# Performance work log

Measured on AMD Instinct MI355X. Metric: run time of the kernel, lower is better.

Reference implementation:

```python
import jax, jax.numpy as jnp
import numpy as np

N_USERS = 200000
N_MOVIES = 80000
N = N_USERS + N_MOVIES
H = 64
F_MOVIE = 20
E = 1250000
EL = 500000


def setup_inputs() -> dict:
    key = jax.random.key(0)
    ks = jax.random.split(key, 13)
    s = 0.05
    inp = {
        "movie_x": jax.random.normal(ks[0], (N_MOVIES, F_MOVIE), jnp.float32),
        "user_emb": jax.random.normal(ks[1], (N_USERS, H), jnp.float32) * s,
        "movie_emb": jax.random.normal(ks[2], (N_MOVIES, H), jnp.float32) * s,
        "lin_W": jax.random.normal(ks[3], (H, F_MOVIE), jnp.float32) * s,
        "lin_b": jax.random.normal(ks[4], (H,), jnp.float32) * s,
        "W1l": jax.random.normal(ks[5], (H, H), jnp.float32) * s,
        "b1": jax.random.normal(ks[6], (H,), jnp.float32) * s,
        "W1r": jax.random.normal(ks[7], (H, H), jnp.float32) * s,
        "W2l": jax.random.normal(ks[8], (H, H), jnp.float32) * s,
        "b2": jax.random.normal(ks[9], (H,), jnp.float32) * s,
        "W2r": jax.random.normal(ks[10], (H, H), jnp.float32) * s,
        "edge_index": jax.random.randint(ks[11], (2, E), 0, N, jnp.int64),
        "edge_label_index": jnp.stack([
            jax.random.randint(jax.random.fold_in(ks[12], 0), (EL,), 0, N_USERS, jnp.int64),
            jax.random.randint(jax.random.fold_in(ks[12], 1), (EL,), 0, N_MOVIES, jnp.int64),
        ]),
    }
    return inp


def _sage(x, src, dst, Wl, bl, Wr):
    # PyG SAGEConv, mean aggregation: lin_l(mean_{j->i} x_j) + lin_r(x_i)
    msg = x[src]  # [E, H] gather
    agg = jax.ops.segment_sum(msg, dst, num_segments=N)  # [N, H] scatter-add
    deg = jax.ops.segment_sum(jnp.ones((src.shape[0],), x.dtype), dst, num_segments=N)
    mean = agg / jnp.maximum(deg, 1.0)[:, None]
    return mean @ Wl.T + bl + x @ Wr.T


def reference(movie_x, user_emb, movie_emb, lin_W, lin_b,
              W1l, b1, W1r, W2l, b2, W2r, edge_index, edge_label_index):
    # encode: users = embedding lookup (node_id == arange), movies = linear(x) + embedding
    x_user = user_emb
    x_movie = movie_x @ lin_W.T + lin_b + movie_emb
    x = jnp.concatenate([x_user, x_movie], axis=0)  # [N, H]

    src, dst = edge_index[0], edge_index[1]
    x = jax.nn.relu(_sage(x, src, dst, W1l, b1, W1r))
    x = _sage(x, src, dst, W2l, b2, W2r)

    xu = x[:N_USERS]
    xm = x[N_USERS:]
    # dot-product edge scoring over supervision edges
    u = xu[edge_label_index[0]]  # [EL, H]
    m = xm[edge_label_index[1]]  # [EL, H]
    return jnp.sum(u * m, axis=-1)  # [EL]
```

## Files before the change

kernel.cpp:

```cpp
#include <hip/hip_runtime.h>
#include <hip/hip_bf16.h>

#define NU 200000
#define NM 80000
#define NT 280000
#define HD 64
#define FM 20

#define BSHIFT 10
#define NBUCK ((NT + 1023) >> 10)
#define SCHUNK 4096
#define UBLK 6250

#define PD 72
#define PD8 (PD / 8)

typedef __attribute__((ext_vector_type(8))) short short8;
typedef __attribute__((ext_vector_type(4))) float floatx4;

__device__ __forceinline__ float bfu2f(unsigned short u) {
    union { unsigned int u; float f; } c; c.u = ((unsigned int)u) << 16; return c.f;
}

__device__ __forceinline__ unsigned short f2bf_raw(float f) {
    union { float f; unsigned int u; } c; c.f = f;
    unsigned int u = c.u + 0x7FFFu + ((c.u >> 16) & 1u);
    return (unsigned short)(u >> 16);
}

__device__ __forceinline__ float ldf(const void* p, long i, int isbf) {
    return isbf ? bfu2f(((const unsigned short*)p)[i]) : ((const float*)p)[i];
}
__device__ __forceinline__ int ldidx(const int* p, long j, int is64) {
    return is64 ? p[2 * j] : p[j];
}

__device__ __forceinline__ int probe_isbf(const void* user_emb, int lane) {
    int bad = 0;
    for (int i = lane; i < 128; i += 64) {
        unsigned short h = ((const unsigned short*)user_emb)[i];
        if (((h >> 7) & 0xFF) >= 135) bad = 1;
    }
    return (__ballot(bad != 0) == 0ULL) ? 1 : 0;
}
__device__ __forceinline__ int probe_is64(const int* ei, int lane) {
    int odd = 0;
    if (lane < 16 && ei[2 * lane + 1] != 0) odd = 1;
    return (__ballot(odd != 0) == 0ULL) ? 1 : 0;
}

__global__ __launch_bounds__(256) void prep_nodes(
    const void* __restrict__ user_emb,
    const void* __restrict__ movie_x,
    const void* __restrict__ movie_emb,
    const void* __restrict__ lin_W,
    const void* __restrict__ lin_b,
    unsigned short* __restrict__ xb)
{
    int tid = threadIdx.x;
    int lane = tid & 63;
    int isbf = probe_isbf(user_emb, lane);

    if (blockIdx.x < UBLK) {
        long t = (long)blockIdx.x * 256 + tid;
        if (isbf) {
            ((short8*)xb)[t] = ((const short8*)user_emb)[t];
        } else {
            floatx4 a = ((const floatx4*)user_emb)[2 * t];
            floatx4 b = ((const floatx4*)user_emb)[2 * t + 1];
            short8 r;
            r[0] = (short)f2bf_raw(a[0]); r[1] = (short)f2bf_raw(a[1]);
            r[2] = (short)f2bf_raw(a[2]); r[3] = (short)f2bf_raw(a[3]);
            r[4] = (short)f2bf_raw(b[0]); r[5] = (short)f2bf_raw(b[1]);
            r[6] = (short)f2bf_raw(b[2]); r[7] = (short)f2bf_raw(b[3]);
            ((short8*)xb)[t] = r;
        }
        return;
    }

    int wave = (blockIdx.x - UBLK) * 4 + (tid >> 6);
    int m0 = __builtin_amdgcn_readfirstlane(wave << 2);
    if (m0 >= NM) return;

    float wr[FM];
    if (isbf) {
        const unsigned int* p = (const unsigned int*)((const unsigned short*)lin_W + (long)lane * FM);
        #pragma unroll
        for (int i = 0; i < FM / 2; ++i) {
            unsigned int u = p[i];
            wr[2 * i]     = bfu2f((unsigned short)(u & 0xFFFFu));
            wr[2 * i + 1] = bfu2f((unsigned short)(u >> 16));
        }
    } else {
        const floatx4* p = (const floatx4*)((const float*)lin_W + (long)lane * FM);
        #pragma unroll
        for (int i = 0; i < FM / 4; ++i) {
            floatx4 v = p[i];
            wr[4 * i] = v[0]; wr[4 * i + 1] = v[1]; wr[4 * i + 2] = v[2]; wr[4 * i + 3] = v[3];
        }
    }
    float bias = ldf(lin_b, lane, isbf);

    #pragma unroll
    for (int mm = 0; mm < 4; ++mm) {
        int m = m0 + mm;
        float a0 = bias + ldf(movie_emb, (long)m * HD + lane, isbf);
        float a1 = 0.f, a2 = 0.f, a3 = 0.f;
        if (isbf) {
            const unsigned int* mr = (const unsigned int*)((const unsigned short*)movie_x + (long)m * FM);
            #pragma unroll
            for (int kk = 0; kk < FM / 2; ++kk) {
                unsigned int u = mr[kk];
                float x0 = bfu2f((unsigned short)(u & 0xFFFFu));
                float x1 = bfu2f((unsigned short)(u >> 16));
                if (kk & 1) { a2 += x0 * wr[2 * kk]; a3 += x1 * wr[2 * kk + 1]; }
                else        { a0 += x0 * wr[2 * kk]; a1 += x1 * wr[2 * kk + 1]; }
            }
        } else {
            const float* mr = (const float*)movie_x + (long)m * FM;
            #pragma unroll
            for (int k = 0; k < FM; k += 4) {
                a0 += mr[k]     * wr[k];
                a1 += mr[k + 1] * wr[k + 1];
                a2 += mr[k + 2] * wr[k + 2];
                a3 += mr[k + 3] * wr[k + 3];
            }
        }
        xb[(long)(NU + m) * HD + lane] = f2bf_raw((a0 + a1) + (a2 + a3));
    }
}

__global__ __launch_bounds__(512) void blk_hist(
    const int* __restrict__ ei, int E,
    int* __restrict__ blkhist)
{
    __shared__ int h[NBUCK];
    int tid = threadIdx.x;
    int is64 = probe_is64(ei, tid & 63);
    for (int i = tid; i < NBUCK; i += 512) h[i] = 0;
    __syncthreads();
    long e0 = (long)blockIdx.x * SCHUNK;
    long e1 = e0 + SCHUNK; if (e1 > E) e1 = E;
    for (long j = e0 + tid; j < e1; j += 512) {
        int d = ldidx(ei, (long)E + j, is64);
        atomicAdd(&h[d >> BSHIFT], 1);
    }
    __syncthreads();
    long obase = (long)blockIdx.x * NBUCK;
    for (int i = tid; i < NBUCK; i += 512) blkhist[obase + i] = h[i];
}

__global__ __launch_bounds__(256) void col_scan(
    int* __restrict__ blkhist, int NSB,
    int* __restrict__ bcnt)
{
    __shared__ int larr[2048];
    __shared__ int lsum[256];
    int b = blockIdx.x;
    int t = threadIdx.x;
    for (int i = t; i < NSB; i += 256) larr[i] = blkhist[(long)i * NBUCK + b];
    __syncthreads();
    int C = (NSB + 255) >> 8;
    int beg = t * C;
    int end = beg + C; if (end > NSB) end = NSB; if (beg > NSB) beg = NSB;
    int s = 0;
    for (int i = beg; i < end; ++i) s += larr[i];
    lsum[t] = s;
    __syncthreads();
    for (int off = 1; off < 256; off <<= 1) {
        int v = lsum[t];
        if (t >= off) v += lsum[t - off];
        __syncthreads();
        lsum[t] = v;
        __syncthreads();
    }
    int run = (t == 0) ? 0 : lsum[t - 1];
    for (int i = beg; i < end; ++i) {
        int v = larr[i];
        blkhist[(long)i * NBUCK + b] = run;
        run += v;
    }
    if (t == 0) bcnt[b] = lsum[255];
}

__global__ __launch_bounds__(512) void scatter_kernel(
    const int* __restrict__ ei, int E,
    const int* __restrict__ bcnt,
    const int* __restrict__ blkhist,
    int* __restrict__ packed)
{
    __shared__ int sscan[512];
    __shared__ int cur[NBUCK];
    int tid = threadIdx.x;
    int is64 = probe_is64(ei, tid & 63);

    sscan[tid] = (tid < NBUCK) ? bcnt[tid] : 0;
    __syncthreads();
    for (int off = 1; off < 512; off <<= 1) {
        int v = sscan[tid];
        if (tid >= off) v += sscan[tid - off];
        __syncthreads();
        sscan[tid] = v;
        __syncthreads();
    }
    long obase = (long)blockIdx.x * NBUCK;
    if (tid < NBUCK) {
        int bs = (tid == 0) ? 0 : sscan[tid - 1];
        cur[tid] = bs + blkhist[obase + tid];
    }
    __syncthreads();

    long e0 = (long)blockIdx.x * SCHUNK;
    long e1 = e0 + SCHUNK; if (e1 > E) e1 = E;
    for (long j = e0 + tid; j < e1; j += 512) {
        int s = ldidx(ei, j, is64);
        int d = ldidx(ei, (long)E + j, is64);
        int b = d >> BSHIFT;
        int pos = atomicAdd(&cur[b], 1);
        packed[pos] = (s << BSHIFT) | (d & ((1 << BSHIFT) - 1));
    }
}

__global__ __launch_bounds__(256) void finefill_kernel(
    const int* __restrict__ bcnt,
    const int* __restrict__ packed,
    int* __restrict__ rowptr,
    int* __restrict__ cnt,
    int* __restrict__ srclist)
{
    __shared__ int lcnt[1 << BSHIFT];
    __shared__ int lsum[256];
    __shared__ int sb[NBUCK + 1];
    int b = blockIdx.x;
    int tid = threadIdx.x;
    int nbase = b << BSHIFT;

    int a0 = (2 * tid     < NBUCK) ? bcnt[2 * tid]     : 0;
    int a1 = (2 * tid + 1 < NBUCK) ? bcnt[2 * tid + 1] : 0;
    lsum[tid] = a0 + a1;
    __syncthreads();
    for (int off = 1; off < 256; off <<= 1) {
        int v = lsum[tid];
        if (tid >= off) v += lsum[tid - off];
        __syncthreads();
        lsum[tid] = v;
        __syncthreads();
    }
    {
        int run = (tid == 0) ? 0 : lsum[tid - 1];
        if (2 * tid     < NBUCK) sb[2 * tid]     = run;
        if (2 * tid + 1 < NBUCK) sb[2 * tid + 1] = run + a0;
        if (tid == 0) sb[NBUCK] = lsum[255];
    }
    for (int i = tid; i < (1 << BSHIFT); i += 256) lcnt[i] = 0;
    __syncthreads();
    int beg = sb[b];
    int end = sb[b + 1];

    for (int j = beg + tid; j < end; j += 256)
        atomicAdd(&lcnt[packed[j] & ((1 << BSHIFT) - 1)], 1);
    __syncthreads();

    int i0 = tid * 4;
    int c0 = lcnt[i0], c1 = lcnt[i0 + 1], c2 = lcnt[i0 + 2], c3 = lcnt[i0 + 3];
    lsum[tid] = c0 + c1 + c2 + c3;
    __syncthreads();
    for (int off = 1; off < 256; off <<= 1) {
        int v = lsum[tid];
        if (tid >= off) v += lsum[tid - off];
        __syncthreads();
        lsum[tid] = v;
        __syncthreads();
    }
    int run = beg + ((tid == 0) ? 0 : lsum[tid - 1]);
    int r0 = run, r1 = r0 + c0, r2 = r1 + c1, r3 = r2 + c2;

    int n0 = nbase + i0;
    if (n0     < NT) { rowptr[n0]     = r0; cnt[n0]     = c0; }
    if (n0 + 1 < NT) { rowptr[n0 + 1] = r1; cnt[n0 + 1] = c1; }
    if (n0 + 2 < NT) { rowptr[n0 + 2] = r2; cnt[n0 + 2] = c2; }
    if (n0 + 3 < NT) { rowptr[n0 + 3] = r3; cnt[n0 + 3] = c3; }

    lcnt[i0] = r0; lcnt[i0 + 1] = r1; lcnt[i0 + 2] = r2; lcnt[i0 + 3] = r3;
    __syncthreads();

    for (int j = beg + tid; j < end; j += 256) {
        int p = packed[j];
        int dl = p & ((1 << BSHIFT) - 1);
        int pos = atomicAdd(&lcnt[dl], 1);
        srclist[pos] = p >> BSHIFT;
    }
}

template <bool RELU>
__global__ __launch_bounds__(512) void sage_layer(
    const unsigned short* __restrict__ xin,
    const int* __restrict__ rowptr,
    const int* __restrict__ cnt,
    const int* __restrict__ srclist,
    const void* __restrict__ Wl,
    const void* __restrict__ bias,
    const void* __restrict__ Wr,
    unsigned short* __restrict__ xout,
    const void* __restrict__ uprobe)
{
    __shared__ short8 lWl8[HD * PD8];
    __shared__ short8 lWr8[HD * PD8];
    __shared__ short8 lm8[HD * PD8];
    __shared__ float lb[HD];

    int tid = threadIdx.x;
    int lane = tid & 63;
    int isbf = probe_isbf(uprobe, lane);

    if (isbf) {
        const short8* wl8 = (const short8*)Wl;
        const short8* wr8 = (const short8*)Wr;
        int i = tid;
        int di = (i >> 3) * PD8 + (i & 7);
        lWl8[di] = wl8[i];
        lWr8[di] = wr8[i];
    } else {
        const floatx4* wlf = (const floatx4*)Wl;
        const floatx4* wrf = (const floatx4*)Wr;
        int i = tid;
        int di = (i >> 3) * PD8 + (i & 7);
        floatx4 a = wlf[2 * i], b = wlf[2 * i + 1];
        short8 r;
        r[0]=(short)f2bf_raw(a[0]); r[1]=(short)f2bf_raw(a[1]); r[2]=(short)f2bf_raw(a[2]); r[3]=(short)f2bf_raw(a[3]);
        r[4]=(short)f2bf_raw(b[0]); r[5]=(short)f2bf_raw(b[1]); r[6]=(short)f2bf_raw(b[2]); r[7]=(short)f2bf_raw(b[3]);
        lWl8[di] = r;
        a = wrf[2 * i]; b = wrf[2 * i + 1];
        r[0]=(short)f2bf_raw(a[0]); r[1]=(short)f2bf_raw(a[1]); r[2]=(short)f2bf_raw(a[2]); r[3]=(short)f2bf_raw(a[3]);
        r[4]=(short)f2bf_raw(b[0]); r[5]=(short)f2bf_raw(b[1]); r[6]=(short)f2bf_raw(b[2]); r[7]=(short)f2bf_raw(b[3]);
        lWr8[di] = r;
    }
    if (tid < HD) lb[tid] = ldf(bias, tid, isbf);

    int tile = blockIdx.x;
    long base = (long)tile * HD * HD;

    int w8 = tid >> 6;
    int mrow = lane & 15;
    int quad = lane >> 4;
    int roww = (w8 & 3) * 16 + mrow;
    int htp  = w8 >> 2;

    const short8* xrow = (const short8*)&xin[base + (long)roww * HD];
    short8 ax0 = xrow[quad];
    short8 ax1 = xrow[quad + 4];

    int g = lane >> 3;
    int sub = lane & 7;
    int nl = w8 * 8 + g;
    int n = tile * 64 + nl;
    int beg = rowptr[n];
    int deg = cnt[n];

    float acc[8];
    #pragma unroll
    for (int k = 0; k < 8; ++k) acc[k] = 0.f;

    for (int j0 = 0; j0 < deg; j0 += 8) {
        int e = j0 + sub;
        int sv = (e < deg) ? srclist[beg + e] : 0;
        int cq = deg - j0; if (cq > 8) cq = 8;
        short8 r[8];
        #pragma unroll
        for (int q = 0; q < 8; ++q) {
            int s = __shfl(sv, (g << 3) | q);
            r[q] = *(const short8*)&xin[(long)s * HD + sub * 8];
        }
        #pragma unroll
        for (int q = 0; q < 8; ++q) {
            if (q < cq) {
                #pragma unroll
                for (int k = 0; k < 8; ++k)
                    acc[k] += bfu2f((unsigned short)r[q][k]);
            }
        }
    }

    float rd = 1.0f / fmaxf((float)deg, 1.0f);
    short8 o;
    #pragma unroll
    for (int k = 0; k < 8; ++k) o[k] = (short)f2bf_raw(acc[k] * rd);
    lm8[nl * PD8 + sub] = o;

    __syncthreads();

    short8 am0 = lm8[roww * PD8 + quad];
    short8 am1 = lm8[roww * PD8 + 4 + quad];

    floatx4 acc4[2];
    #pragma unroll
    for (int t = 0; t < 2; ++t) {
        int h = (htp * 2 + t) * 16 + mrow;
        short8 bl0 = lWl8[h * PD8 + quad];
        short8 bl1 = lWl8[h * PD8 + 4 + quad];
        short8 br0 = lWr8[h * PD8 + quad];
        short8 br1 = lWr8[h * PD8 + 4 + quad];
        floatx4 a = {0.f, 0.f, 0.f, 0.f};
        a = __builtin_amdgcn_mfma_f32_16x16x32_bf16(am0, bl0, a, 0, 0, 0);
        a = __builtin_amdgcn_mfma_f32_16x16x32_bf16(am1, bl1, a, 0, 0, 0);
        a = __builtin_amdgcn_mfma_f32_16x16x32_bf16(ax0, br0, a, 0, 0, 0);
        a = __builtin_amdgcn_mfma_f32_16x16x32_bf16(ax1, br1, a, 0, 0, 0);
        acc4[t] = a;
    }

    #pragma unroll
    for (int t = 0; t < 2; ++t) {
        int h = (htp * 2 + t) * 16 + mrow;
        float bv = lb[h];
        #pragma unroll
        for (int r = 0; r < 4; ++r) {
            int node = (w8 & 3) * 16 + quad * 4 + r;
            float v = acc4[t][r] + bv;
            if (RELU) v = fmaxf(v, 0.0f);
            xout[base + node * HD + h] = f2bf_raw(v);
        }
    }
}

__global__ __launch_bounds__(256) void dot_kernel(
    const unsigned short* __restrict__ x2,
    const int* __restrict__ eli,
    void* __restrict__ out,
    int EL,
    const int* __restrict__ ei,
    const void* __restrict__ uprobe)
{
    int lane = threadIdx.x & 63;
    int isbf = probe_isbf(uprobe, lane);
    int is64 = probe_is64(ei, lane);

    int wid = (blockIdx.x * 256 + threadIdx.x) >> 6;
    long base = (long)wid * 32;
    if (base >= EL) return;

    int idxv = (lane < 32) ? ldidx(eli, base + lane, is64)
                           : ldidx(eli, (long)EL + base + (lane - 32), is64);

    int e   = lane >> 2;
    int seg = lane & 3;
    int uA = __shfl(idxv, e);
    int uB = __shfl(idxv, e + 16);
    int mA = __shfl(idxv, 32 + e);
    int mB = __shfl(idxv, 48 + e);

    const short8* upA = (const short8*)(x2 + (long)uA * HD + seg * 16);
    const short8* mpA = (const short8*)(x2 + (long)(NU + mA) * HD + seg * 16);
    const short8* upB = (const short8*)(x2 + (long)uB * HD + seg * 16);
    const short8* mpB = (const short8*)(x2 + (long)(NU + mB) * HD + seg * 16);
    short8 a0 = upA[0], a1 = upA[1];
    short8 b0 = mpA[0], b1 = mpA[1];
    short8 c0 = upB[0], c1 = upB[1];
    short8 d0 = mpB[0], d1 = mpB[1];

    float pA = 0.f, pB = 0.f;
    #pragma unroll
    for (int j = 0; j < 8; ++j) {
        pA += bfu2f((unsigned short)a0[j]) * bfu2f((unsigned short)b0[j]);
        pA += bfu2f((unsigned short)a1[j]) * bfu2f((unsigned short)b1[j]);
        pB += bfu2f((unsigned short)c0[j]) * bfu2f((unsigned short)d0[j]);
        pB += bfu2f((unsigned short)c1[j]) * bfu2f((unsigned short)d1[j]);
    }
    pA += __shfl_xor(pA, 1);
    pA += __shfl_xor(pA, 2);
    pB += __shfl_xor(pB, 1);
    pB += __shfl_xor(pB, 2);

    if (seg == 0) {
        long gA = base + e;
        long gB = base + e + 16;
        if (isbf) {
            ((unsigned short*)out)[gA] = f2bf_raw(pA);
            ((unsigned short*)out)[gB] = f2bf_raw(pB);
        } else {
            ((float*)out)[gA] = pA;
            ((float*)out)[gB] = pB;
        }
    }
}

extern "C" void kernel_launch(void* const* d_in, const int* in_sizes, int n_in,
                              void* d_out, int out_size, void* d_ws, size_t ws_size,
                              hipStream_t stream)
{
    const void* movie_x   = d_in[0];
    const void* user_emb  = d_in[1];
    const void* movie_emb = d_in[2];
    const void* lin_W     = d_in[3];
    const void* lin_b     = d_in[4];
    const void* W1l       = d_in[5];
    const void* b1        = d_in[6];
    const void* W1r       = d_in[7];
    const void* W2l       = d_in[8];
    const void* b2        = d_in[9];
    const void* W2r       = d_in[10];
    const int* ei  = (const int*)d_in[11];
    const int* eli = (const int*)d_in[12];
    int E  = in_sizes[11] / 2;
    int EL = in_sizes[12] / 2;

    const int NSB = (E + SCHUNK - 1) / SCHUNK;

    char* w = (char*)d_ws;
    unsigned short* xb0     = (unsigned short*)w;  w += (size_t)NT * HD * 2;
    unsigned short* xb1     = (unsigned short*)w;  w += (size_t)NT * HD * 2;
    int*            cnt     = (int*)w;             w += (size_t)NT * 4;
    int*            rowptr  = (int*)w;             w += (size_t)NT * 4;
    int*            srclist = (int*)w;             w += (size_t)E * 4;
    int*            packed  = (int*)w;             w += (size_t)E * 4;
    int*            bcnt    = (int*)w;             w += (size_t)(NBUCK + 1) * 4;
    int*            blkhist = (int*)w;             w += (size_t)NSB * NBUCK * 4;

    const int node_blocks   = UBLK + NM / 16;
    const int tile_blocks   = NT / 64;
    const int dot_blocks    = ((EL + 31) / 32 + 3) / 4;

    prep_nodes<<<node_blocks, 256, 0, stream>>>(user_emb, movie_x, movie_emb, lin_W, lin_b, xb0);

    blk_hist<<<NSB, 512, 0, stream>>>(ei, E, blkhist);
    col_scan<<<NBUCK, 256, 0, stream>>>(blkhist, NSB, bcnt);
    scatter_kernel<<<NSB, 512, 0, stream>>>(ei, E, bcnt, blkhist, packed);
    finefill_kernel<<<NBUCK, 256, 0, stream>>>(bcnt, packed, rowptr, cnt, srclist);

    sage_layer<true><<<tile_blocks, 512, 0, stream>>>(xb0, rowptr, cnt, srclist, W1l, b1, W1r, xb1, user_emb);
    sage_layer<false><<<tile_blocks, 512, 0, stream>>>(xb1, rowptr, cnt, srclist, W2l, b2, W2r, xb0, user_emb);

    dot_kernel<<<dot_blocks, 256, 0, stream>>>(xb0, eli, d_out, EL, ei, user_emb);
}
```

Baseline: 302.4 us.

## Stage scatter through LDS for coalesced writes, compute dtype flags once

After: 293.3 us. 3.0% less time.

```diff
diff --git a/kernel.cpp b/kernel.cpp
--- a/kernel.cpp
+++ b/kernel.cpp
@@ -17,6 +17,8 @@
 
 typedef __attribute__((ext_vector_type(8))) short short8;
 typedef __attribute__((ext_vector_type(4))) float floatx4;
+typedef __attribute__((ext_vector_type(4))) unsigned int uint4v;
+typedef __attribute__((ext_vector_type(2))) float float2v;
 
 __device__ __forceinline__ float bfu2f(unsigned short u) {
     union { unsigned int u; float f; } c; c.u = ((unsigned int)u) << 16; return c.f;
@@ -33,20 +35,6 @@
 }
 __device__ __forceinline__ int ldidx(const int* p, long j, int is64) {
     return is64 ? p[2 * j] : p[j];
-}
-
-__device__ __forceinline__ int probe_isbf(const void* user_emb, int lane) {
-    int bad = 0;
-    for (int i = lane; i < 128; i += 64) {
-        unsigned short h = ((const unsigned short*)user_emb)[i];
-        if (((h >> 7) & 0xFF) >= 135) bad = 1;
-    }
-    return (__ballot(bad != 0) == 0ULL) ? 1 : 0;
-}
-__device__ __forceinline__ int probe_is64(const int* ei, int lane) {
-    int odd = 0;
-    if (lane < 16 && ei[2 * lane + 1] != 0) odd = 1;
-    return (__ballot(odd != 0) == 0ULL) ? 1 : 0;
 }
 
 __global__ __launch_bounds__(256) void prep_nodes(
@@ -55,11 +43,26 @@
     const void* __restrict__ movie_emb,
     const void* __restrict__ lin_W,
     const void* __restrict__ lin_b,
-    unsigned short* __restrict__ xb)
+    const int* __restrict__ ei,
+    unsigned short* __restrict__ xb,
+    int* __restrict__ flags)
 {
     int tid = threadIdx.x;
     int lane = tid & 63;
-    int isbf = probe_isbf(user_emb, lane);
+
+    int bad = 0;
+    for (int i = lane; i < 128; i += 64) {
+        unsigned short h = ((const unsigned short*)user_emb)[i];
+        if (((h >> 7) & 0xFF) >= 135) bad = 1;
+    }
+    int isbf = (__ballot(bad != 0) == 0ULL) ? 1 : 0;
+
+    if (blockIdx.x == 0 && tid < 64) {
+        int odd = 0;
+        if (lane < 16 && ei[2 * lane + 1] != 0) odd = 1;
+        int is64 = (__ballot(odd != 0) == 0ULL) ? 1 : 0;
+        if (lane == 0) { flags[0] = isbf; flags[1] = is64; }
+    }
 
     if (blockIdx.x < UBLK) {
         long t = (long)blockIdx.x * 256 + tid;
@@ -132,11 +135,12 @@
 
 __global__ __launch_bounds__(512) void blk_hist(
     const int* __restrict__ ei, int E,
-    int* __restrict__ blkhist)
+    int* __restrict__ blkhist,
+    const int* __restrict__ flags)
 {
     __shared__ int h[NBUCK];
     int tid = threadIdx.x;
-    int is64 = probe_is64(ei, tid & 63);
+    int is64 = flags[1];
     for (int i = tid; i < NBUCK; i += 512) h[i] = 0;
     __syncthreads();
     long e0 = (long)blockIdx.x * SCHUNK;
@@ -187,12 +191,35 @@
     const int* __restrict__ ei, int E,
     const int* __restrict__ bcnt,
     const int* __restrict__ blkhist,
-    int* __restrict__ packed)
+    int* __restrict__ packed,
+    const int* __restrict__ flags)
 {
     __shared__ int sscan[512];
-    __shared__ int cur[NBUCK];
+    __shared__ int gb[NBUCK];
+    __shared__ int lbase[NBUCK];
+    __shared__ int lcur[NBUCK];
+    __shared__ int lpk[SCHUNK];
+    __shared__ short lbk[SCHUNK];
+
     int tid = threadIdx.x;
-    int is64 = probe_is64(ei, tid & 63);
+    int is64 = flags[1];
+    long e0 = (long)blockIdx.x * SCHUNK;
+    int n = (int)(((long)E - e0 < SCHUNK) ? ((long)E - e0) : SCHUNK);
+
+    for (int i = tid; i < NBUCK; i += 512) lcur[i] = 0;
+    __syncthreads();
+
+    int s[8], d[8];
+    #pragma unroll
+    for (int k = 0; k < 8; ++k) {
+        int j = tid + k * 512;
+        if (j < n) {
+            s[k] = ldidx(ei, e0 + j, is64);
+            d[k] = ldidx(ei, (long)E + e0 + j, is64);
+            atomicAdd(&lcur[d[k] >> BSHIFT], 1);
+        }
+    }
+    __syncthreads();
 
     sscan[tid] = (tid < NBUCK) ? bcnt[tid] : 0;
     __syncthreads();
@@ -204,20 +231,42 @@
         __syncthreads();
     }
     long obase = (long)blockIdx.x * NBUCK;
+    if (tid < NBUCK)
+        gb[tid] = ((tid == 0) ? 0 : sscan[tid - 1]) + blkhist[obase + tid];
+    __syncthreads();
+
+    int c = (tid < NBUCK) ? lcur[tid] : 0;
+    sscan[tid] = c;
+    __syncthreads();
+    for (int off = 1; off < 512; off <<= 1) {
+        int v = sscan[tid];
+        if (tid >= off) v += sscan[tid - off];
+        __syncthreads();
+        sscan[tid] = v;
+        __syncthreads();
+    }
     if (tid < NBUCK) {
-        int bs = (tid == 0) ? 0 : sscan[tid - 1];
-        cur[tid] = bs + blkhist[obase + tid];
-    }
-    __syncthreads();
-
-    long e0 = (long)blockIdx.x * SCHUNK;
-    long e1 = e0 + SCHUNK; if (e1 > E) e1 = E;
-    for (long j = e0 + tid; j < e1; j += 512) {
-        int s = ldidx(ei, j, is64);
-        int d = ldidx(ei, (long)E + j, is64);
-        int b = d >> BSHIFT;
-        int pos = atomicAdd(&cur[b], 1);
-        packed[pos] = (s << BSHIFT) | (d & ((1 << BSHIFT) - 1));
+        int ex = (tid == 0) ? 0 : sscan[tid - 1];
+        lbase[tid] = ex;
+        lcur[tid] = ex;
+    }
+    __syncthreads();
+
+    #pragma unroll
+    for (int k = 0; k < 8; ++k) {
+        int j = tid + k * 512;
+        if (j < n) {
+            int b = d[k] >> BSHIFT;
+            int pos = atomicAdd(&lcur[b], 1);
+            lpk[pos] = (s[k] << BSHIFT) | (d[k] & ((1 << BSHIFT) - 1));
+            lbk[pos] = (short)b;
+        }
+    }
+    __syncthreads();
+
+    for (int i = tid; i < n; i += 512) {
+        int b = lbk[i];
+        packed[gb[b] + (i - lbase[b])] = lpk[i];
     }
 }
 
@@ -302,7 +351,7 @@
     const void* __restrict__ bias,
     const void* __restrict__ Wr,
     unsigned short* __restrict__ xout,
-    const void* __restrict__ uprobe)
+    const int* __restrict__ flags)
 {
     __shared__ short8 lWl8[HD * PD8];
     __shared__ short8 lWr8[HD * PD8];
@@ -310,8 +359,7 @@
     __shared__ float lb[HD];
 
     int tid = threadIdx.x;
-    int lane = tid & 63;
-    int isbf = probe_isbf(uprobe, lane);
+    int isbf = flags[0];
 
     if (isbf) {
         const short8* wl8 = (const short8*)Wl;
@@ -341,6 +389,7 @@
     long base = (long)tile * HD * HD;
 
     int w8 = tid >> 6;
+    int lane = tid & 63;
     int mrow = lane & 15;
     int quad = lane >> 4;
     int roww = (w8 & 3) * 16 + mrow;
@@ -357,26 +406,32 @@
     int beg = rowptr[n];
     int deg = cnt[n];
 
-    float acc[8];
-    #pragma unroll
-    for (int k = 0; k < 8; ++k) acc[k] = 0.f;
+    float2v acc2[4];
+    #pragma unroll
+    for (int k = 0; k < 4; ++k) { acc2[k][0] = 0.f; acc2[k][1] = 0.f; }
 
     for (int j0 = 0; j0 < deg; j0 += 8) {
         int e = j0 + sub;
         int sv = (e < deg) ? srclist[beg + e] : 0;
         int cq = deg - j0; if (cq > 8) cq = 8;
-        short8 r[8];
+        uint4v r[8];
         #pragma unroll
         for (int q = 0; q < 8; ++q) {
             int s = __shfl(sv, (g << 3) | q);
-            r[q] = *(const short8*)&xin[(long)s * HD + sub * 8];
+            r[q] = *(const uint4v*)&xin[(long)s * HD + sub * 8];
         }
         #pragma unroll
         for (int q = 0; q < 8; ++q) {
             if (q < cq) {
                 #pragma unroll
-                for (int k = 0; k < 8; ++k)
-                    acc[k] += bfu2f((unsigned short)r[q][k]);
+                for (int w = 0; w < 4; ++w) {
+                    unsigned int u = r[q][w];
+                    union { unsigned int u; float f; } lo, hi;
+                    lo.u = u << 16;
+                    hi.u = u & 0xFFFF0000u;
+                    float2v t; t[0] = lo.f; t[1] = hi.f;
+                    acc2[w] += t;
+                }
             }
         }
     }
@@ -384,7 +439,10 @@
     float rd = 1.0f / fmaxf((float)deg, 1.0f);
     short8 o;
     #pragma unroll
-    for (int k = 0; k < 8; ++k) o[k] = (short)f2bf_raw(acc[k] * rd);
+    for (int w = 0; w < 4; ++w) {
+        o[2 * w]     = (short)f2bf_raw(acc2[w][0] * rd);
+        o[2 * w + 1] = (short)f2bf_raw(acc2[w][1] * rd);
+    }
     lm8[nl * PD8 + sub] = o;
 
     __syncthreads();
@@ -427,16 +485,14 @@
     const int* __restrict__ eli,
     void* __restrict__ out,
     int EL,
-    const int* __restrict__ ei,
-    const void* __restrict__ uprobe)
-{
-    int lane = threadIdx.x & 63;
-    int isbf = probe_isbf(uprobe, lane);
-    int is64 = probe_is64(ei, lane);
-
+    const int* __restrict__ flags)
+{
     int wid = (blockIdx.x * 256 + threadIdx.x) >> 6;
     long base = (long)wid * 32;
     if (base >= EL) return;
+    int lane = threadIdx.x & 63;
+    int isbf = flags[0];
+    int is64 = flags[1];
 
     int idxv = (lane < 32) ? ldidx(eli, base + lane, is64)
                            : ldidx(eli, (long)EL + base + (lane - 32), is64);
@@ -514,20 +570,21 @@
     int*            packed  = (int*)w;             w += (size_t)E * 4;
     int*            bcnt    = (int*)w;             w += (size_t)(NBUCK + 1) * 4;
     int*            blkhist = (int*)w;             w += (size_t)NSB * NBUCK * 4;
+    int*            flags   = (int*)w;
 
     const int node_blocks   = UBLK + NM / 16;
     const int tile_blocks   = NT / 64;
     const int dot_blocks    = ((EL + 31) / 32 + 3) / 4;
 
-    prep_nodes<<<node_blocks, 256, 0, stream>>>(user_emb, movie_x, movie_emb, lin_W, lin_b, xb0);
-
-    blk_hist<<<NSB, 512, 0, stream>>>(ei, E, blkhist);
+    prep_nodes<<<node_blocks, 256, 0, stream>>>(user_emb, movie_x, movie_emb, lin_W, lin_b, ei, xb0, flags);
+
+    blk_hist<<<NSB, 512, 0, stream>>>(ei, E, blkhist, flags);
     col_scan<<<NBUCK, 256, 0, stream>>>(blkhist, NSB, bcnt);
-    scatter_kernel<<<NSB, 512, 0, stream>>>(ei, E, bcnt, blkhist, packed);
+    scatter_kernel<<<NSB, 512, 0, stream>>>(ei, E, bcnt, blkhist, packed, flags);
     finefill_kernel<<<NBUCK, 256, 0, stream>>>(bcnt, packed, rowptr, cnt, srclist);
 
-    sage_layer<true><<<tile_blocks, 512, 0, stream>>>(xb0, rowptr, cnt, srclist, W1l, b1, W1r, xb1, user_emb);
-    sage_layer<false><<<tile_blocks, 512, 0, stream>>>(xb1, rowptr, cnt, srclist, W2l, b2, W2r, xb0, user_emb);
-
-    dot_kernel<<<dot_blocks, 256, 0, stream>>>(xb0, eli, d_out, EL, ei, user_emb);
-}
+    sage_layer<true><<<tile_blocks, 512, 0, stream>>>(xb0, rowptr, cnt, srclist, W1l, b1, W1r, xb1, flags);
+    sage_layer<false><<<tile_blocks, 512, 0, stream>>>(xb1, rowptr, cnt, srclist, W2l, b2, W2r, xb0, flags);
+
+    dot_kernel<<<dot_blocks, 256, 0, stream>>>(xb0, eli, d_out, EL, flags);
+}
```
